# Kernel optimization log

Measured on AMD Instinct MI355X. Metric: run time of the kernel, lower is better.

Reference implementation:

```python
import jax, jax.numpy as jnp
import numpy as np

BS, SEQ, C = 8, 1024, 1024

def setup_inputs() -> dict:
    key = jax.random.key(0)
    ks = jax.random.split(key, 5)
    inp = {
        "input": jax.random.normal(ks[0], (BS, SEQ, C), dtype=jnp.float32),
        "Wq": jax.random.normal(ks[1], (C, C), dtype=jnp.float32) * 0.001,
        "Wk": jax.random.normal(ks[2], (C, C), dtype=jnp.float32) * 0.001,
        "Wv": jax.random.normal(ks[3], (C, C), dtype=jnp.float32) * 0.001,
        "bq": jnp.zeros((C,), dtype=jnp.float32),
        "bk": jnp.zeros((C,), dtype=jnp.float32),
        "bv": jnp.zeros((C,), dtype=jnp.float32),
        "bias_position": jnp.ones((SEQ, SEQ), dtype=jnp.float32),
    }
    return inp

def reference(input, Wq, Wk, Wv, bq, bk, bv, bias_position):
    # Linear layers (torch nn.Linear: x @ W.T + b)
    q = input @ Wq.T + bq                      # (bs, seq, c)
    k = input @ Wk.T + bk                      # (bs, seq, c)
    v = input @ Wv.T + bv                      # (bs, seq, c)
    # AFT: out[b,t,c] = sum_s exp(k[b,s,c] + bias[t,s]) * v[b,s,c]
    #                 / sum_s exp(k[b,s,c] + bias[t,s])
    # Factor exp(k + bias) = exp(bias) * exp(k) -> two GEMM-like einsums,
    # avoiding the (seq, bs, seq, c) intermediate of the original.
    ek = jnp.exp(k)                            # (bs, seq, c)
    eb = jnp.exp(bias_position)                # (t, s)
    numerator = jnp.einsum('ts,bsc->btc', eb, ek * v)   # (bs, t, c)
    denominator = jnp.einsum('ts,bsc->btc', eb, ek)     # (bs, t, c)
    out = jax.nn.sigmoid(q) * (numerator / denominator)
    return out
```

## Files before the change

### kernel.cpp

```cpp
#include <hip/hip_runtime.h>

#define BSZ 8
#define SEQL 1024
#define CHN 1024
#define M1 (BSZ*SEQL)

typedef __attribute__((ext_vector_type(8))) short bf16x8;
typedef __attribute__((ext_vector_type(4))) float f32x4;
typedef __attribute__((ext_vector_type(4))) unsigned short us4;
typedef __attribute__((ext_vector_type(8))) unsigned short us8;

static __device__ __forceinline__ unsigned short f2bf(float f){
  unsigned int u = __float_as_uint(f);
  u += 0x7fffu + ((u >> 16) & 1u);
  return (unsigned short)(u >> 16);
}
static __device__ __forceinline__ float bf2f(unsigned short h){
  return __uint_as_float(((unsigned int)h) << 16);
}
static __device__ __forceinline__ void gload16(const void* g, void* l){
  __builtin_amdgcn_global_load_lds((const __attribute__((address_space(1))) void*)g,
                                   (__attribute__((address_space(3))) void*)l,
                                   16, 0, 0);
}

#define SBAR() do { __builtin_amdgcn_sched_barrier(0); __builtin_amdgcn_s_barrier(); __builtin_amdgcn_sched_barrier(0); } while (0)
#define LGKM0() asm volatile("s_waitcnt lgkmcnt(0)" ::: "memory")
#define PRIO_HI() do { __builtin_amdgcn_s_setprio(1); __builtin_amdgcn_sched_barrier(0); } while (0)
#define PRIO_LO() do { __builtin_amdgcn_sched_barrier(0); __builtin_amdgcn_s_setprio(0); } while (0)

__global__ void prep_kernel(const float* __restrict__ x, const float* __restrict__ wq,
                            const float* __restrict__ wk, const float* __restrict__ wv,
                            const float* __restrict__ bias,
                            unsigned short* __restrict__ xb, unsigned short* __restrict__ wqb,
                            unsigned short* __restrict__ wkb, unsigned short* __restrict__ wvb,
                            unsigned short* __restrict__ ebb)
{
  const int NX = M1 * CHN;
  const int NW = CHN * CHN;
  const int total4 = (NX + 3 * NW + SEQL * SEQL) >> 2;
  for (int i = blockIdx.x * blockDim.x + threadIdx.x; i < total4;
       i += gridDim.x * blockDim.x) {
    int e = i << 2;
    const float* src; unsigned short* dst; int off; bool ex = false;
    if (e < NX)               { src = x;    dst = xb;  off = e; }
    else if (e < NX + NW)     { src = wq;   dst = wqb; off = e - NX; }
    else if (e < NX + 2 * NW) { src = wk;   dst = wkb; off = e - (NX + NW); }
    else if (e < NX + 3 * NW) { src = wv;   dst = wvb; off = e - (NX + 2 * NW); }
    else                      { src = bias; dst = ebb; off = e - (NX + 3 * NW); ex = true; }
    float4 v = *reinterpret_cast<const float4*>(src + off);
    if (ex) { v.x = expf(v.x); v.y = expf(v.y); v.z = expf(v.z); v.w = expf(v.w); }
    us4 o; o.x = f2bf(v.x); o.y = f2bf(v.y); o.z = f2bf(v.z); o.w = f2bf(v.w);
    *reinterpret_cast<us4*>(dst + off) = o;
  }
}

__global__ __launch_bounds__(512, 2) void gemm_qkv(
    const unsigned short* __restrict__ Xb,
    const unsigned short* __restrict__ Wq, const unsigned short* __restrict__ Wk,
    const unsigned short* __restrict__ Wv,
    const float* __restrict__ bq, const float* __restrict__ bk,
    const float* __restrict__ bv,
    unsigned short* __restrict__ Qb,
    unsigned short* __restrict__ EKT, unsigned short* __restrict__ EKVT)
{
  __shared__ unsigned short lds[2 * 28672];
  const int tid = threadIdx.x;
  const int lane = tid & 63;
  const int wid = tid >> 6;
  const int wm = wid >> 1;
  const int wn = wid & 1;
  const int nwg = gridDim.x;
  const int lid = blockIdx.x;
  const int sid = (lid & 7) * (nwg >> 3) + (lid >> 3);
  const int m0 = (sid >> 4) * 256;
  const int n0 = (sid & 15) * 64;

  const unsigned short* srcA[4]; int dA[4];
#pragma unroll
  for (int p = 0; p < 4; p++) {
    int l = p * 8192 + tid * 16;
    int row = l >> 7;
    int lc = ((l >> 4) & 7) ^ (row & 7);
    srcA[p] = Xb + (m0 + row) * CHN + lc * 8;
    dA[p] = l >> 1;
  }
  const unsigned short* srcB[3]; int dB[3];
  {
    int l = tid * 16;
    int row = l >> 7;
    int lc = ((l >> 4) & 7) ^ (row & 7);
#pragma unroll
    for (int w = 0; w < 3; w++) {
      const unsigned short* W = (w == 0) ? Wq : (w == 1) ? Wk : Wv;
      srcB[w] = W + (n0 + row) * CHN + lc * 8;
      dB[w] = 16384 + w * 4096 + (l >> 1);
    }
  }

  int aOff[4][2], bOff[2][2];
#pragma unroll
  for (int mi = 0; mi < 4; mi++) {
    int r = wm * 64 + mi * 16 + (lane & 15);
#pragma unroll
    for (int ks = 0; ks < 2; ks++)
      aOff[mi][ks] = r * 64 + ((((ks << 2) + (lane >> 4)) ^ (r & 7)) << 3);
  }
#pragma unroll
  for (int ni = 0; ni < 2; ni++) {
    int r = wn * 32 + ni * 16 + (lane & 15);
#pragma unroll
    for (int ks = 0; ks < 2; ks++)
      bOff[ni][ks] = r * 64 + ((((ks << 2) + (lane >> 4)) ^ (r & 7)) << 3);
  }

  f32x4 accq[4][2] = {}, acck[4][2] = {}, accv[4][2] = {};

#pragma unroll
  for (int p = 0; p < 4; p++) gload16(srcA[p], lds + dA[p]);
#pragma unroll
  for (int w = 0; w < 3; w++) gload16(srcB[w], lds + dB[w]);

  for (int t = 0; t < 16; ++t) {
    const int cur = (t & 1) * 28672;
    const int nxt = 28672 - cur;
    const int kn = (t + 1) << 6;
    if (t < 15) {
#pragma unroll
      for (int p = 0; p < 4; p++) gload16(srcA[p] + kn, lds + nxt + dA[p]);
      asm volatile("s_waitcnt vmcnt(4)" ::: "memory");
    } else {
      asm volatile("s_waitcnt vmcnt(0)" ::: "memory");
    }
    SBAR();
#pragma unroll
    for (int ks = 0; ks < 2; ks++) {
      bf16x8 bqf[2], bkf[2], bvf[2];
#pragma unroll
      for (int ni = 0; ni < 2; ni++) {
        bqf[ni] = *reinterpret_cast<const bf16x8*>(lds + cur + 16384 + bOff[ni][ks]);
        bkf[ni] = *reinterpret_cast<const bf16x8*>(lds + cur + 20480 + bOff[ni][ks]);
        bvf[ni] = *reinterpret_cast<const bf16x8*>(lds + cur + 24576 + bOff[ni][ks]);
      }
      PRIO_HI();
#pragma unroll
      for (int mi = 0; mi < 4; mi++) {
        bf16x8 af = *reinterpret_cast<const bf16x8*>(lds + cur + aOff[mi][ks]);
#pragma unroll
        for (int ni = 0; ni < 2; ni++) {
          accq[mi][ni] = __builtin_amdgcn_mfma_f32_16x16x32_bf16(af, bqf[ni], accq[mi][ni], 0, 0, 0);
          acck[mi][ni] = __builtin_amdgcn_mfma_f32_16x16x32_bf16(af, bkf[ni], acck[mi][ni], 0, 0, 0);
          accv[mi][ni] = __builtin_amdgcn_mfma_f32_16x16x32_bf16(af, bvf[ni], accv[mi][ni], 0, 0, 0);
        }
      }
      PRIO_LO();
      if (ks == 0 && t < 15) {
#pragma unroll
        for (int w = 0; w < 3; w++) gload16(srcB[w] + kn, lds + nxt + dB[w]);
      }
    }
    LGKM0();
    SBAR();
  }

  const int bIdx = m0 >> 10;
  const int s0 = m0 & 1023;
  const int rbq = (lane >> 4) * 4;
  float bqv[2], bkv[2], bvv[2];
#pragma unroll
  for (int ni = 0; ni < 2; ni++) {
    int c = n0 + wn * 32 + ni * 16 + (lane & 15);
    bqv[ni] = bq[c]; bkv[ni] = bk[c]; bvv[ni] = bv[c];
  }
#pragma unroll
  for (int mi = 0; mi < 4; mi++)
#pragma unroll
    for (int ni = 0; ni < 2; ni++) {
      int col = n0 + wn * 32 + ni * 16 + (lane & 15);
#pragma unroll
      for (int r = 0; r < 4; r++) {
        int mrow = m0 + wm * 64 + mi * 16 + rbq + r;
        Qb[mrow * CHN + col] = f2bf(accq[mi][ni][r] + bqv[ni]);
        float ekf = expf(acck[mi][ni][r] + bkv[ni]);
        acck[mi][ni][r] = ekf;
        accv[mi][ni][r] = ekf * (accv[mi][ni][r] + bvv[ni]);
      }
    }
#pragma unroll
  for (int mi = 0; mi < 4; mi++)
#pragma unroll
    for (int ni = 0; ni < 2; ni++) {
      int nloc = wn * 32 + ni * 16 + (lane & 15);
#pragma unroll
      for (int r = 0; r < 4; r++)
        lds[nloc * 264 + wm * 64 + mi * 16 + rbq + r] = f2bf(acck[mi][ni][r]);
    }
  __syncthreads();
#pragma unroll
  for (int it = 0; it < 4; it++) {
    int ch = it * 512 + tid;
    int nloc = ch >> 5, c8 = ch & 31;
    us8 v = *reinterpret_cast<const us8*>(lds + nloc * 264 + c8 * 8);
    *reinterpret_cast<us8*>(EKT + (bIdx * CHN + n0 + nloc) * SEQL + s0 + c8 * 8) = v;
  }
  __syncthreads();
#pragma unroll
  for (int mi = 0; mi < 4; mi++)
#pragma unroll
    for (int ni = 0; ni < 2; ni++) {
      int nloc = wn * 32 + ni * 16 + (lane & 15);
#pragma unroll
      for (int r = 0; r < 4; r++)
        lds[nloc * 264 + wm * 64 + mi * 16 + rbq + r] = f2bf(accv[mi][ni][r]);
    }
  __syncthreads();
#pragma unroll
  for (int it = 0; it < 4; it++) {
    int ch = it * 512 + tid;
    int nloc = ch >> 5, c8 = ch & 31;
    us8 v = *reinterpret_cast<const us8*>(lds + nloc * 264 + c8 * 8);
    *reinterpret_cast<us8*>(EKVT + (bIdx * CHN + n0 + nloc) * SEQL + s0 + c8 * 8) = v;
  }
}

__global__ __launch_bounds__(512, 2) void gemm_aft(
    const unsigned short* __restrict__ EB,
    const unsigned short* __restrict__ EKT, const unsigned short* __restrict__ EKVT,
    const unsigned short* __restrict__ Qb, float* __restrict__ out)
{
  __shared__ unsigned short lds[2 * 32768];
  const int tid = threadIdx.x;
  const int lane = tid & 63;
  const int wid = tid >> 6;
  const int wm = wid >> 2;
  const int wn = wid & 3;
  const int nwg = gridDim.x;
  const int lid = blockIdx.x;
  const int sid = (lid & 7) * (nwg >> 3) + (lid >> 3);
  const int t0 = (sid & 3) * 256;
  const int n0 = (sid >> 2) * 128;

  const unsigned short* srcA[4]; int dA[4];
#pragma unroll
  for (int p = 0; p < 4; p++) {
    int l = p * 8192 + tid * 16;
    int row = l >> 7;
    int lc = ((l >> 4) & 7) ^ (row & 7);
    srcA[p] = EB + (t0 + row) * SEQL + lc * 8;
    dA[p] = l >> 1;
  }
  const unsigned short* srcB[2][2]; int dB[2][2];
#pragma unroll
  for (int w = 0; w < 2; w++) {
    const unsigned short* B = (w == 0) ? EKT : EKVT;
#pragma unroll
    for (int p = 0; p < 2; p++) {
      int l = p * 8192 + tid * 16;
      int row = l >> 7;
      int lc = ((l >> 4) & 7) ^ (row & 7);
      srcB[w][p] = B + (n0 + row) * SEQL + lc * 8;
      dB[w][p] = 16384 + w * 8192 + (l >> 1);
    }
  }

  int aOff[8][2], bOff[2][2];
#pragma unroll
  for (int mi = 0; mi < 8; mi++) {
    int r = wm * 128 + mi * 16 + (lane & 15);
#pragma unroll
    for (int ks = 0; ks < 2; ks++)
      aOff[mi][ks] = r * 64 + ((((ks << 2) + (lane >> 4)) ^ (r & 7)) << 3);
  }
#pragma unroll
  for (int ni = 0; ni < 2; ni++) {
    int r = wn * 32 + ni * 16 + (lane & 15);
#pragma unroll
    for (int ks = 0; ks < 2; ks++)
      bOff[ni][ks] = r * 64 + ((((ks << 2) + (lane >> 4)) ^ (r & 7)) << 3);
  }

  f32x4 accd[8][2] = {}, accn[8][2] = {};

#pragma unroll
  for (int p = 0; p < 4; p++) gload16(srcA[p], lds + dA[p]);
#pragma unroll
  for (int w = 0; w < 2; w++)
#pragma unroll
    for (int p = 0; p < 2; p++) gload16(srcB[w][p], lds + dB[w][p]);

  for (int t = 0; t < 16; ++t) {
    const int cur = (t & 1) * 32768;
    const int nxt = 32768 - cur;
    const int kn = (t + 1) << 6;
    if (t < 15) {
#pragma unroll
      for (int p = 0; p < 4; p++) gload16(srcA[p] + kn, lds + nxt + dA[p]);
      asm volatile("s_waitcnt vmcnt(4)" ::: "memory");
    } else {
      asm volatile("s_waitcnt vmcnt(0)" ::: "memory");
    }
    SBAR();
#pragma unroll
    for (int ks = 0; ks < 2; ks++) {
      bf16x8 bdf[2], bnf[2];
#pragma unroll
      for (int ni = 0; ni < 2; ni++) {
        bdf[ni] = *reinterpret_cast<const bf16x8*>(lds + cur + 16384 + bOff[ni][ks]);
        bnf[ni] = *reinterpret_cast<const bf16x8*>(lds + cur + 24576 + bOff[ni][ks]);
      }
      PRIO_HI();
#pragma unroll
      for (int mi = 0; mi < 8; mi++) {
        bf16x8 af = *reinterpret_cast<const bf16x8*>(lds + cur + aOff[mi][ks]);
#pragma unroll
        for (int ni = 0; ni < 2; ni++) {
          accd[mi][ni] = __builtin_amdgcn_mfma_f32_16x16x32_bf16(af, bdf[ni], accd[mi][ni], 0, 0, 0);
          accn[mi][ni] = __builtin_amdgcn_mfma_f32_16x16x32_bf16(af, bnf[ni], accn[mi][ni], 0, 0, 0);
        }
      }
      PRIO_LO();
      if (ks == 0 && t < 15) {
#pragma unroll
        for (int w = 0; w < 2; w++)
#pragma unroll
          for (int p = 0; p < 2; p++) gload16(srcB[w][p] + kn, lds + nxt + dB[w][p]);
      }
    }
    LGKM0();
    SBAR();
  }

  const int rbq = (lane >> 4) * 4;
#pragma unroll
  for (int mi = 0; mi < 8; mi++)
#pragma unroll
    for (int ni = 0; ni < 2; ni++) {
      int nloc = wn * 32 + ni * 16 + (lane & 15);
      int n = n0 + nloc;
      int b = n >> 10, c = n & 1023;
#pragma unroll
      for (int r = 0; r < 4; r++) {
        int tt = t0 + wm * 128 + mi * 16 + rbq + r;
        float qv = bf2f(Qb[(b * SEQL + tt) * CHN + c]);
        float sig = 1.0f / (1.0f + expf(-qv));
        out[(b * SEQL + tt) * CHN + c] = sig * accn[mi][ni][r] / accd[mi][ni][r];
      }
    }
}

extern "C" void kernel_launch(void* const* d_in, const int* in_sizes, int n_in,
                              void* d_out, int out_size, void* d_ws, size_t ws_size,
                              hipStream_t stream) {
  (void)in_sizes; (void)n_in; (void)out_size; (void)ws_size;
  const float* x    = (const float*)d_in[0];
  const float* wq   = (const float*)d_in[1];
  const float* wk   = (const float*)d_in[2];
  const float* wv   = (const float*)d_in[3];
  const float* bq   = (const float*)d_in[4];
  const float* bk   = (const float*)d_in[5];
  const float* bv   = (const float*)d_in[6];
  const float* bias = (const float*)d_in[7];
  float* out = (float*)d_out;

  char* ws = (char*)d_ws;
  const size_t MB = 1024 * 1024;
  unsigned short* Xb   = (unsigned short*)(ws);
  unsigned short* Wqb  = (unsigned short*)(ws + 16 * MB);
  unsigned short* Wkb  = (unsigned short*)(ws + 18 * MB);
  unsigned short* Wvb  = (unsigned short*)(ws + 20 * MB);
  unsigned short* EBb  = (unsigned short*)(ws + 22 * MB);
  unsigned short* Qb   = (unsigned short*)(ws + 24 * MB);
  unsigned short* EKT  = (unsigned short*)(ws + 40 * MB);
  unsigned short* EKVT = (unsigned short*)(ws + 56 * MB);

  prep_kernel<<<2048, 256, 0, stream>>>(x, wq, wk, wv, bias, Xb, Wqb, Wkb, Wvb, EBb);
  gemm_qkv<<<512, 512, 0, stream>>>(Xb, Wqb, Wkb, Wvb, bq, bk, bv, Qb, EKT, EKVT);
  gemm_aft<<<256, 512, 0, stream>>>(EBb, EKT, EKVT, Qb, out);
}
```

Measured before the change: 189.9 us.

## Retile both GEMMs with BK=32 and smaller tiles, doubling AFT grid

Both GEMM kernels move from a 64-wide K step to a 32-wide K step with a 4-chunk XOR swizzle, which shrinks LDS buffers. gemm_qkv changes its block tile from 256x64 to 128x128 with a 2x4 wave grid, and gemm_aft changes from 256x128 to 256x64 tiles, doubling its grid to 512 workgroups. All fragment loads are issued up front, followed by an explicit lgkmcnt wait before the MFMA block. The intent is better occupancy and better load balance across CUs. The cost is twice as many K iterations and barriers, less data reuse per tile, and lower arithmetic intensity in the AFT kernel.

```diff
diff --git a/kernel.cpp b/kernel.cpp
--- a/kernel.cpp
+++ b/kernel.cpp
@@ -23,9 +23,10 @@
                                    (__attribute__((address_space(3))) void*)l,
                                    16, 0, 0);
 }
+static __device__ __forceinline__ int s4(int r){ return (r & 3) ^ ((r >> 2) & 3); }
 
 #define SBAR() do { __builtin_amdgcn_sched_barrier(0); __builtin_amdgcn_s_barrier(); __builtin_amdgcn_sched_barrier(0); } while (0)
-#define LGKM0() asm volatile("s_waitcnt lgkmcnt(0)" ::: "memory")
+#define LGKM0() do { asm volatile("s_waitcnt lgkmcnt(0)" ::: "memory"); __builtin_amdgcn_sched_barrier(0); } while (0)
 #define PRIO_HI() do { __builtin_amdgcn_s_setprio(1); __builtin_amdgcn_sched_barrier(0); } while (0)
 #define PRIO_LO() do { __builtin_amdgcn_sched_barrier(0); __builtin_amdgcn_s_setprio(0); } while (0)
 
@@ -64,102 +65,81 @@
     unsigned short* __restrict__ Qb,
     unsigned short* __restrict__ EKT, unsigned short* __restrict__ EKVT)
 {
-  __shared__ unsigned short lds[2 * 28672];
+  __shared__ unsigned short lds[2 * 16384];
   const int tid = threadIdx.x;
   const int lane = tid & 63;
   const int wid = tid >> 6;
-  const int wm = wid >> 1;
-  const int wn = wid & 1;
-  const int nwg = gridDim.x;
+  const int wm = wid >> 2;
+  const int wn = wid & 3;
   const int lid = blockIdx.x;
-  const int sid = (lid & 7) * (nwg >> 3) + (lid >> 3);
-  const int m0 = (sid >> 4) * 256;
-  const int n0 = (sid & 15) * 64;
-
-  const unsigned short* srcA[4]; int dA[4];
-#pragma unroll
-  for (int p = 0; p < 4; p++) {
-    int l = p * 8192 + tid * 16;
-    int row = l >> 7;
-    int lc = ((l >> 4) & 7) ^ (row & 7);
-    srcA[p] = Xb + (m0 + row) * CHN + lc * 8;
-    dA[p] = l >> 1;
-  }
-  const unsigned short* srcB[3]; int dB[3];
-  {
-    int l = tid * 16;
-    int row = l >> 7;
-    int lc = ((l >> 4) & 7) ^ (row & 7);
-#pragma unroll
-    for (int w = 0; w < 3; w++) {
-      const unsigned short* W = (w == 0) ? Wq : (w == 1) ? Wk : Wv;
-      srcB[w] = W + (n0 + row) * CHN + lc * 8;
-      dB[w] = 16384 + w * 4096 + (l >> 1);
-    }
-  }
-
-  int aOff[4][2], bOff[2][2];
+  const int sid = (lid & 7) * 64 + (lid >> 3);
+  const int m0 = (sid & 63) * 128;
+  const int n0 = (sid >> 6) * 128;
+
+  const int srow = tid >> 2, sc = tid & 3;
+  const int scol = ((sc ^ s4(srow)) * 8);
+  const unsigned short* gA = Xb + (m0 + srow) * CHN + scol;
+  const unsigned short* gB0 = Wq + (n0 + srow) * CHN + scol;
+  const unsigned short* gB1 = Wk + (n0 + srow) * CHN + scol;
+  const unsigned short* gB2 = Wv + (n0 + srow) * CHN + scol;
+  const int dA = tid * 8;
+  const int dB = 4096 + tid * 8;
+
+  int aOff[4], bOff[2];
+  const int c0 = lane >> 4;
 #pragma unroll
   for (int mi = 0; mi < 4; mi++) {
     int r = wm * 64 + mi * 16 + (lane & 15);
-#pragma unroll
-    for (int ks = 0; ks < 2; ks++)
-      aOff[mi][ks] = r * 64 + ((((ks << 2) + (lane >> 4)) ^ (r & 7)) << 3);
+    aOff[mi] = r * 32 + (c0 ^ s4(r)) * 8;
   }
 #pragma unroll
   for (int ni = 0; ni < 2; ni++) {
     int r = wn * 32 + ni * 16 + (lane & 15);
-#pragma unroll
-    for (int ks = 0; ks < 2; ks++)
-      bOff[ni][ks] = r * 64 + ((((ks << 2) + (lane >> 4)) ^ (r & 7)) << 3);
+    bOff[ni] = r * 32 + (c0 ^ s4(r)) * 8;
   }
 
   f32x4 accq[4][2] = {}, acck[4][2] = {}, accv[4][2] = {};
 
-#pragma unroll
-  for (int p = 0; p < 4; p++) gload16(srcA[p], lds + dA[p]);
-#pragma unroll
-  for (int w = 0; w < 3; w++) gload16(srcB[w], lds + dB[w]);
-
-  for (int t = 0; t < 16; ++t) {
-    const int cur = (t & 1) * 28672;
-    const int nxt = 28672 - cur;
-    const int kn = (t + 1) << 6;
-    if (t < 15) {
-#pragma unroll
-      for (int p = 0; p < 4; p++) gload16(srcA[p] + kn, lds + nxt + dA[p]);
+  gload16(gA, lds + dA);
+  gload16(gB0, lds + dB);
+  gload16(gB1, lds + dB + 4096);
+  gload16(gB2, lds + dB + 8192);
+
+  for (int j = 0; j < 32; ++j) {
+    const int cur = (j & 1) * 16384;
+    const int nxt = 16384 - cur;
+    const int kn = (j + 1) << 5;
+    if (j < 31) {
+      gload16(gA + kn, lds + nxt + dA);
+      gload16(gB0 + kn, lds + nxt + dB);
+      gload16(gB1 + kn, lds + nxt + dB + 4096);
+      gload16(gB2 + kn, lds + nxt + dB + 8192);
       asm volatile("s_waitcnt vmcnt(4)" ::: "memory");
     } else {
       asm volatile("s_waitcnt vmcnt(0)" ::: "memory");
     }
     SBAR();
-#pragma unroll
-    for (int ks = 0; ks < 2; ks++) {
-      bf16x8 bqf[2], bkf[2], bvf[2];
+    bf16x8 af[4], bqf[2], bkf[2], bvf[2];
+#pragma unroll
+    for (int mi = 0; mi < 4; mi++)
+      af[mi] = *reinterpret_cast<const bf16x8*>(lds + cur + aOff[mi]);
+#pragma unroll
+    for (int ni = 0; ni < 2; ni++) {
+      bqf[ni] = *reinterpret_cast<const bf16x8*>(lds + cur + 4096  + bOff[ni]);
+      bkf[ni] = *reinterpret_cast<const bf16x8*>(lds + cur + 8192  + bOff[ni]);
+      bvf[ni] = *reinterpret_cast<const bf16x8*>(lds + cur + 12288 + bOff[ni]);
+    }
+    LGKM0();
+    PRIO_HI();
+#pragma unroll
+    for (int mi = 0; mi < 4; mi++)
 #pragma unroll
       for (int ni = 0; ni < 2; ni++) {
-        bqf[ni] = *reinterpret_cast<const bf16x8*>(lds + cur + 16384 + bOff[ni][ks]);
-        bkf[ni] = *reinterpret_cast<const bf16x8*>(lds + cur + 20480 + bOff[ni][ks]);
-        bvf[ni] = *reinterpret_cast<const bf16x8*>(lds + cur + 24576 + bOff[ni][ks]);
+        accq[mi][ni] = __builtin_amdgcn_mfma_f32_16x16x32_bf16(af[mi], bqf[ni], accq[mi][ni], 0, 0, 0);
+        acck[mi][ni] = __builtin_amdgcn_mfma_f32_16x16x32_bf16(af[mi], bkf[ni], acck[mi][ni], 0, 0, 0);
+        accv[mi][ni] = __builtin_amdgcn_mfma_f32_16x16x32_bf16(af[mi], bvf[ni], accv[mi][ni], 0, 0, 0);
       }
-      PRIO_HI();
-#pragma unroll
-      for (int mi = 0; mi < 4; mi++) {
-        bf16x8 af = *reinterpret_cast<const bf16x8*>(lds + cur + aOff[mi][ks]);
-#pragma unroll
-        for (int ni = 0; ni < 2; ni++) {
-          accq[mi][ni] = __builtin_amdgcn_mfma_f32_16x16x32_bf16(af, bqf[ni], accq[mi][ni], 0, 0, 0);
-          acck[mi][ni] = __builtin_amdgcn_mfma_f32_16x16x32_bf16(af, bkf[ni], acck[mi][ni], 0, 0, 0);
-          accv[mi][ni] = __builtin_amdgcn_mfma_f32_16x16x32_bf16(af, bvf[ni], accv[mi][ni], 0, 0, 0);
-        }
-      }
-      PRIO_LO();
-      if (ks == 0 && t < 15) {
-#pragma unroll
-        for (int w = 0; w < 3; w++) gload16(srcB[w] + kn, lds + nxt + dB[w]);
-      }
-    }
-    LGKM0();
+    PRIO_LO();
     SBAR();
   }
 
@@ -193,14 +173,14 @@
       int nloc = wn * 32 + ni * 16 + (lane & 15);
 #pragma unroll
       for (int r = 0; r < 4; r++)
-        lds[nloc * 264 + wm * 64 + mi * 16 + rbq + r] = f2bf(acck[mi][ni][r]);
+        lds[nloc * 136 + wm * 64 + mi * 16 + rbq + r] = f2bf(acck[mi][ni][r]);
     }
   __syncthreads();
 #pragma unroll
   for (int it = 0; it < 4; it++) {
     int ch = it * 512 + tid;
-    int nloc = ch >> 5, c8 = ch & 31;
-    us8 v = *reinterpret_cast<const us8*>(lds + nloc * 264 + c8 * 8);
+    int nloc = ch >> 4, c8 = ch & 15;
+    us8 v = *reinterpret_cast<const us8*>(lds + nloc * 136 + c8 * 8);
     *reinterpret_cast<us8*>(EKT + (bIdx * CHN + n0 + nloc) * SEQL + s0 + c8 * 8) = v;
   }
   __syncthreads();
@@ -211,14 +191,14 @@
       int nloc = wn * 32 + ni * 16 + (lane & 15);
 #pragma unroll
       for (int r = 0; r < 4; r++)
-        lds[nloc * 264 + wm * 64 + mi * 16 + rbq + r] = f2bf(accv[mi][ni][r]);
+        lds[nloc * 136 + wm * 64 + mi * 16 + rbq + r] = f2bf(accv[mi][ni][r]);
     }
   __syncthreads();
 #pragma unroll
   for (int it = 0; it < 4; it++) {
     int ch = it * 512 + tid;
-    int nloc = ch >> 5, c8 = ch & 31;
-    us8 v = *reinterpret_cast<const us8*>(lds + nloc * 264 + c8 * 8);
+    int nloc = ch >> 4, c8 = ch & 15;
+    us8 v = *reinterpret_cast<const us8*>(lds + nloc * 136 + c8 * 8);
     *reinterpret_cast<us8*>(EKVT + (bIdx * CHN + n0 + nloc) * SEQL + s0 + c8 * 8) = v;
   }
 }
@@ -228,111 +208,85 @@
     const unsigned short* __restrict__ EKT, const unsigned short* __restrict__ EKVT,
     const unsigned short* __restrict__ Qb, float* __restrict__ out)
 {
-  __shared__ unsigned short lds[2 * 32768];
+  __shared__ unsigned short lds[2 * 12288];
   const int tid = threadIdx.x;
   const int lane = tid & 63;
   const int wid = tid >> 6;
-  const int wm = wid >> 2;
-  const int wn = wid & 3;
-  const int nwg = gridDim.x;
+  const int wm = wid >> 1;
+  const int wn = wid & 1;
   const int lid = blockIdx.x;
-  const int sid = (lid & 7) * (nwg >> 3) + (lid >> 3);
+  const int sid = (lid & 7) * 64 + (lid >> 3);
   const int t0 = (sid & 3) * 256;
-  const int n0 = (sid >> 2) * 128;
-
-  const unsigned short* srcA[4]; int dA[4];
-#pragma unroll
-  for (int p = 0; p < 4; p++) {
-    int l = p * 8192 + tid * 16;
-    int row = l >> 7;
-    int lc = ((l >> 4) & 7) ^ (row & 7);
-    srcA[p] = EB + (t0 + row) * SEQL + lc * 8;
-    dA[p] = l >> 1;
-  }
-  const unsigned short* srcB[2][2]; int dB[2][2];
-#pragma unroll
-  for (int w = 0; w < 2; w++) {
-    const unsigned short* B = (w == 0) ? EKT : EKVT;
-#pragma unroll
-    for (int p = 0; p < 2; p++) {
-      int l = p * 8192 + tid * 16;
-      int row = l >> 7;
-      int lc = ((l >> 4) & 7) ^ (row & 7);
-      srcB[w][p] = B + (n0 + row) * SEQL + lc * 8;
-      dB[w][p] = 16384 + w * 8192 + (l >> 1);
-    }
-  }
-
-  int aOff[8][2], bOff[2][2];
-#pragma unroll
-  for (int mi = 0; mi < 8; mi++) {
-    int r = wm * 128 + mi * 16 + (lane & 15);
-#pragma unroll
-    for (int ks = 0; ks < 2; ks++)
-      aOff[mi][ks] = r * 64 + ((((ks << 2) + (lane >> 4)) ^ (r & 7)) << 3);
+  const int n0 = (sid >> 2) * 64;
+
+  const int ar0 = tid >> 2, ac0 = tid & 3;
+  const int ar1 = (tid + 512) >> 2, ac1 = tid & 3;
+  const unsigned short* gA0 = EB + (t0 + ar0) * SEQL + (ac0 ^ s4(ar0)) * 8;
+  const unsigned short* gA1 = EB + (t0 + ar1) * SEQL + (ac1 ^ s4(ar1)) * 8;
+  const int dA0 = tid * 8, dA1 = (tid + 512) * 8;
+  const int bw = tid >> 8;
+  const int bch = tid & 255;
+  const int brow = bch >> 2, bc = bch & 3;
+  const unsigned short* gB = (bw ? EKVT : EKT) + (n0 + brow) * SEQL + (bc ^ s4(brow)) * 8;
+  const int dB = 8192 + bw * 2048 + bch * 8;
+
+  int aOff[4], bOff[2];
+  const int c0 = lane >> 4;
+#pragma unroll
+  for (int mi = 0; mi < 4; mi++) {
+    int r = wm * 64 + mi * 16 + (lane & 15);
+    aOff[mi] = r * 32 + (c0 ^ s4(r)) * 8;
   }
 #pragma unroll
   for (int ni = 0; ni < 2; ni++) {
     int r = wn * 32 + ni * 16 + (lane & 15);
-#pragma unroll
-    for (int ks = 0; ks < 2; ks++)
-      bOff[ni][ks] = r * 64 + ((((ks << 2) + (lane >> 4)) ^ (r & 7)) << 3);
-  }
-
-  f32x4 accd[8][2] = {}, accn[8][2] = {};
-
-#pragma unroll
-  for (int p = 0; p < 4; p++) gload16(srcA[p], lds + dA[p]);
-#pragma unroll
-  for (int w = 0; w < 2; w++)
-#pragma unroll
-    for (int p = 0; p < 2; p++) gload16(srcB[w][p], lds + dB[w][p]);
-
-  for (int t = 0; t < 16; ++t) {
-    const int cur = (t & 1) * 32768;
-    const int nxt = 32768 - cur;
-    const int kn = (t + 1) << 6;
-    if (t < 15) {
-#pragma unroll
-      for (int p = 0; p < 4; p++) gload16(srcA[p] + kn, lds + nxt + dA[p]);
-      asm volatile("s_waitcnt vmcnt(4)" ::: "memory");
+    bOff[ni] = r * 32 + (c0 ^ s4(r)) * 8;
+  }
+
+  f32x4 accd[4][2] = {}, accn[4][2] = {};
+
+  gload16(gA0, lds + dA0);
+  gload16(gA1, lds + dA1);
+  gload16(gB, lds + dB);
+
+  for (int j = 0; j < 32; ++j) {
+    const int cur = (j & 1) * 12288;
+    const int nxt = 12288 - cur;
+    const int kn = (j + 1) << 5;
+    if (j < 31) {
+      gload16(gA0 + kn, lds + nxt + dA0);
+      gload16(gA1 + kn, lds + nxt + dA1);
+      gload16(gB + kn, lds + nxt + dB);
+      asm volatile("s_waitcnt vmcnt(3)" ::: "memory");
     } else {
       asm volatile("s_waitcnt vmcnt(0)" ::: "memory");
     }
     SBAR();
-#pragma unroll
-    for (int ks = 0; ks < 2; ks++) {
-      bf16x8 bdf[2], bnf[2];
+    bf16x8 af[4], bdf[2], bnf[2];
+#pragma unroll
+    for (int mi = 0; mi < 4; mi++)
+      af[mi] = *reinterpret_cast<const bf16x8*>(lds + cur + aOff[mi]);
+#pragma unroll
+    for (int ni = 0; ni < 2; ni++) {
+      bdf[ni] = *reinterpret_cast<const bf16x8*>(lds + cur + 8192  + bOff[ni]);
+      bnf[ni] = *reinterpret_cast<const bf16x8*>(lds + cur + 10240 + bOff[ni]);
+    }
+    LGKM0();
+    PRIO_HI();
+#pragma unroll
+    for (int mi = 0; mi < 4; mi++)
 #pragma unroll
       for (int ni = 0; ni < 2; ni++) {
-        bdf[ni] = *reinterpret_cast<const bf16x8*>(lds + cur + 16384 + bOff[ni][ks]);
-        bnf[ni] = *reinterpret_cast<const bf16x8*>(lds + cur + 24576 + bOff[ni][ks]);
+        accd[mi][ni] = __builtin_amdgcn_mfma_f32_16x16x32_bf16(af[mi], bdf[ni], accd[mi][ni], 0, 0, 0);
+        accn[mi][ni] = __builtin_amdgcn_mfma_f32_16x16x32_bf16(af[mi], bnf[ni], accn[mi][ni], 0, 0, 0);
       }
-      PRIO_HI();
-#pragma unroll
-      for (int mi = 0; mi < 8; mi++) {
-        bf16x8 af = *reinterpret_cast<const bf16x8*>(lds + cur + aOff[mi][ks]);
-#pragma unroll
-        for (int ni = 0; ni < 2; ni++) {
-          accd[mi][ni] = __builtin_amdgcn_mfma_f32_16x16x32_bf16(af, bdf[ni], accd[mi][ni], 0, 0, 0);
-          accn[mi][ni] = __builtin_amdgcn_mfma_f32_16x16x32_bf16(af, bnf[ni], accn[mi][ni], 0, 0, 0);
-        }
-      }
-      PRIO_LO();
-      if (ks == 0 && t < 15) {
-#pragma unroll
-        for (int w = 0; w < 2; w++)
-#pragma unroll
-          for (int p = 0; p < 2; p++) gload16(srcB[w][p] + kn, lds + nxt + dB[w][p]);
-      }
-    }
-    LGKM0();
+    PRIO_LO();
     SBAR();
   }
 
   const int rbq = (lane >> 4) * 4;
 #pragma unroll
-  for (int mi = 0; mi < 8; mi++)
+  for (int mi = 0; mi < 4; mi++)
 #pragma unroll
     for (int ni = 0; ni < 2; ni++) {
       int nloc = wn * 32 + ni * 16 + (lane & 15);
@@ -340,7 +294,7 @@
       int b = n >> 10, c = n & 1023;
 #pragma unroll
       for (int r = 0; r < 4; r++) {
-        int tt = t0 + wm * 128 + mi * 16 + rbq + r;
+        int tt = t0 + wm * 64 + mi * 16 + rbq + r;
         float qv = bf2f(Qb[(b * SEQL + tt) * CHN + c]);
         float sig = 1.0f / (1.0f + expf(-qv));
         out[(b * SEQL + tt) * CHN + c] = sig * accn[mi][ni][r] / accd[mi][ni][r];
@@ -375,5 +329,5 @@
 
   prep_kernel<<<2048, 256, 0, stream>>>(x, wq, wk, wv, bias, Xb, Wqb, Wkb, Wvb, EBb);
   gemm_qkv<<<512, 512, 0, stream>>>(Xb, Wqb, Wkb, Wvb, bq, bk, bv, Qb, EKT, EKVT);
-  gemm_aft<<<256, 512, 0, stream>>>(EBb, EKT, EKVT, Qb, out);
-}
+  gemm_aft<<<512, 512, 0, stream>>>(EBb, EKT, EKVT, Qb, out);
+}
```

Measured after the change: 204.7 us. 1.08x slower.
